# Kernel tuning notes

Measured on AMD Instinct MI355X. Metric: run time of the kernel, lower is better.

The kernel has to match this reference:

```python
import jax, jax.numpy as jnp
import numpy as np

BETA = 25.0  # torch nn.Softplus(beta=25.0)

def softplus_b(z):
    return jax.nn.softplus(BETA * z) / BETA

def setup_inputs() -> dict:
    key = jax.random.key(0)
    ks = jax.random.split(key, 9)
    B, H = 16384, 512
    def lin_init(kw, kb, out_f, in_f):
        bound = 1.0 / np.sqrt(in_f)
        W = jax.random.uniform(kw, (out_f, in_f), jnp.float32, -bound, bound)
        b = jax.random.uniform(kb, (out_f,), jnp.float32, -bound, bound)
        return W, b
    W0, b0 = lin_init(ks[1], ks[2], H, 4)
    W1, b1 = lin_init(ks[3], ks[4], H, H)
    W2, b2 = lin_init(ks[5], ks[6], H, H)
    W3, b3 = lin_init(ks[7], ks[8], 5, H)
    x = jax.random.normal(ks[0], (B, 4), jnp.float32)
    return {"x": x, "W0": W0, "b0": b0, "W1": W1, "b1": b1,
            "W2": W2, "b2": b2, "W3": W3, "b3": b3}

def reference(x, W0, b0, W1, b1, W2, b2, W3, b3):
    def net(z):  # (4,) -> (5,)
        h = softplus_b(W0 @ z + b0)
        h = softplus_b(W1 @ h + b1)
        h = softplus_b(W2 @ h + b2)
        return W3 @ h + b3

    def A_matrix(z):  # antisymmetrized Jacobian of first 4 outputs, (4,4)
        J = jax.jacrev(lambda p: net(p)[:4])(z)
        return J - J.T

    def point_trace(z):
        # T[i,j,k] = d A[i,j] / d z[k]; torch einsum('...ii') -> sum_j T[i,j,j]
        T = jax.jacfwd(A_matrix)(z)  # (4,4,4)
        return jnp.einsum('ijj->i', T)  # (4,)

    trace = jax.vmap(point_trace)(x)          # (B,4)
    u = jax.vmap(net)(x)                      # (B,5)
    return jnp.concatenate([trace, u[:, 4:5]], axis=1)  # (B,5)
```

## Files before the change

kernel.cpp:

```cpp
#include <hip/hip_runtime.h>
#include <math.h>

#define HDIM 512
#define NCH 16
#define BETA 25.0f
#define KV 1536

typedef unsigned short ushort_t;
typedef __attribute__((ext_vector_type(8))) short short8;
typedef __attribute__((ext_vector_type(4))) float f32x4;

__device__ __forceinline__ ushort_t f2bf(float f) {
    unsigned u = __float_as_uint(f);
    unsigned r = (u + 0x7fff + ((u >> 16) & 1)) >> 16;
    return (ushort_t)r;
}
__device__ __forceinline__ float bf2f(ushort_t b) {
    return __uint_as_float(((unsigned)b) << 16);
}
__device__ __forceinline__ void split_bf(float v, ushort_t& hi, ushort_t& lo) {
    hi = f2bf(v);
    lo = f2bf(v - bf2f(hi));
}

__device__ __forceinline__ void softplus_jet(float v, float& phi, float& s, float& pp) {
    float y = BETA * v;
    float e = expf(-fabsf(y));
    float inv = 1.0f / (1.0f + e);
    s = (y >= 0.0f) ? inv : e * inv;
    phi = (fmaxf(y, 0.0f) + log1pf(e)) * (1.0f / BETA);
    pp = BETA * s * (1.0f - s);
}

__device__ __forceinline__ void gl_lds16(const void* g, void* l) {
    __builtin_amdgcn_global_load_lds(
        (const __attribute__((address_space(1))) unsigned int*)g,
        (__attribute__((address_space(3))) unsigned int*)l, 16, 0, 0);
}

__global__ __launch_bounds__(256) void layer0_jet(
    const float* __restrict__ x, const float* __restrict__ W0,
    const float* __restrict__ b0, ushort_t* __restrict__ A0)
{
    __shared__ ushort_t sm[16 * 1024];
    int p = blockIdx.x, tid = threadIdx.x;
    float4 z = *reinterpret_cast<const float4*>(&x[p * 4]);
#pragma unroll
    for (int half = 0; half < 2; ++half) {
        int n = half * 256 + tid;
        float4 w = *reinterpret_cast<const float4*>(&W0[n * 4]);
        float v = fmaf(w.x, z.x, fmaf(w.y, z.y, fmaf(w.z, z.z, fmaf(w.w, z.w, b0[n]))));
        float phi, s, pp;
        softplus_jet(v, phi, s, pp);
        float wa[4] = {w.x, w.y, w.z, w.w};
        float o[16];
        o[0] = phi;
#pragma unroll
        for (int a = 0; a < 4; ++a) o[1 + a] = s * wa[a];
        int idx = 5;
#pragma unroll
        for (int a = 0; a < 4; ++a)
#pragma unroll
            for (int b = a; b < 4; ++b) { o[idx] = pp * wa[a] * wa[b]; ++idx; }
        o[15] = 0.0f;
#pragma unroll
        for (int c = 0; c < 16; ++c) {
            ushort_t hb, lb;
            split_bf(o[c], hb, lb);
            sm[c * 1024 + n] = hb;
            sm[c * 1024 + 512 + n] = lb;
        }
    }
    __syncthreads();
    uint4* d4 = reinterpret_cast<uint4*>(A0 + (size_t)p * 16 * 1024);
    const uint4* s4 = reinterpret_cast<const uint4*>(sm);
#pragma unroll
    for (int i = 0; i < 8; ++i) d4[tid + 256 * i] = s4[tid + 256 * i];
}

template<int EPI>
__global__ __launch_bounds__(256, 2) void gemm_jet(
    const ushort_t* __restrict__ Ag, const ushort_t* __restrict__ BT,
    const float* __restrict__ bias, ushort_t* __restrict__ Anext,
    float* __restrict__ Sout)
{
    __shared__ char smem[32768];
    ushort_t* Al = (ushort_t*)smem;
    ushort_t* Bl = (ushort_t*)(smem + 16384);
    float*    epi = (float*)smem;

    const int tid = threadIdx.x, wave = tid >> 6, lane = tid & 63;

    int nwg = gridDim.x;
    int bid = blockIdx.x;
    int q = nwg >> 3, r = nwg & 7;
    int xcd = bid & 7, i8 = bid >> 3;
    int logical = (xcd < r ? xcd * (q + 1) : r * (q + 1) + (xcd - r) * q) + i8;
    const int m0 = (logical >> 2) * 128;
    const int n0 = (logical & 3) * 128;
    const int wm = (wave >> 1) * 64, wn = (wave & 1) * 64;

    f32x4 acc[4][4] = {};

    const int sr = wave * 32 + (lane >> 3);
    const int sc = (lane & 7) * 8;

    for (int t = 0; t < KV / 64; ++t) {
        int k0 = t * 64;
        int ka = (k0 < 512) ? k0 : k0 - 512;
        __syncthreads();
#pragma unroll
        for (int i = 0; i < 4; ++i)
            gl_lds16(Ag + (size_t)(m0 + sr + i * 8) * 1024 + ka + sc,
                     Al + (wave * 32 + i * 8) * 64);
#pragma unroll
        for (int i = 0; i < 4; ++i)
            gl_lds16(BT + (size_t)(n0 + sr + i * 8) * KV + k0 + sc,
                     Bl + (wave * 32 + i * 8) * 64);
        __syncthreads();
        const int rA = lane & 15;
#pragma unroll
        for (int kk = 0; kk < 2; ++kk) {
            const int kc = kk * 32 + (lane >> 4) * 8;
            short8 af[4], bf[4];
#pragma unroll
            for (int mi = 0; mi < 4; ++mi)
                af[mi] = *(const short8*)&Al[(wm + mi * 16 + rA) * 64 + kc];
#pragma unroll
            for (int ni = 0; ni < 4; ++ni)
                bf[ni] = *(const short8*)&Bl[(wn + ni * 16 + rA) * 64 + kc];
#pragma unroll
            for (int mi = 0; mi < 4; ++mi)
#pragma unroll
                for (int ni = 0; ni < 4; ++ni)
                    acc[mi][ni] = __builtin_amdgcn_mfma_f32_16x16x32_bf16(
                        af[mi], bf[ni], acc[mi][ni], 0, 0, 0);
        }
    }

    const int pl = lane & 15, ph = lane >> 4;
#pragma unroll
    for (int h = 0; h < 2; ++h) {
        __syncthreads();
        if ((wave >> 1) == h) {
#pragma unroll
            for (int mi = 0; mi < 4; ++mi)
#pragma unroll
                for (int ni = 0; ni < 4; ++ni)
#pragma unroll
                    for (int rr = 0; rr < 4; ++rr)
                        epi[(mi * 16 + ph * 4 + rr) * 128 + wn + ni * 16 + pl] = acc[mi][ni][rr];
        }
        __syncthreads();
#pragma unroll
        for (int rep = 0; rep < 2; ++rep) {
            int idx = rep * 256 + tid;
            int n = idx & 127, pq = idx >> 7;
            const float* vp = &epi[pq * 16 * 128 + n];
            float v[15];
#pragma unroll
            for (int c = 0; c < 15; ++c) v[c] = vp[c * 128];
            float val = v[0] + bias[n0 + n];
            float phi, s, pp;
            softplus_jet(val, phi, s, pp);
            float o[16];
            o[0] = phi;
            float d[4];
#pragma unroll
            for (int a = 0; a < 4; ++a) { d[a] = v[1 + a]; o[1 + a] = s * d[a]; }
            int ix = 5;
#pragma unroll
            for (int a = 0; a < 4; ++a)
#pragma unroll
                for (int b = a; b < 4; ++b) { o[ix] = pp * d[a] * d[b] + s * v[ix]; ++ix; }
            o[15] = 0.0f;
            size_t prow = (size_t)(m0 >> 4) + h * 4 + pq;
            if (EPI == 1) {
                size_t rb = prow * 16 * 1024;
#pragma unroll
                for (int c = 0; c < 16; ++c) {
                    ushort_t hb, lb;
                    split_bf(o[c], hb, lb);
                    Anext[rb + (size_t)c * 1024 + n0 + n] = hb;
                    Anext[rb + (size_t)c * 1024 + 512 + n0 + n] = lb;
                }
            } else {
                float4* op = reinterpret_cast<float4*>(Sout + ((size_t)prow * 512 + n0 + n) * 16);
#pragma unroll
                for (int qq = 0; qq < 4; ++qq)
                    op[qq] = make_float4(o[4*qq], o[4*qq+1], o[4*qq+2], o[4*qq+3]);
            }
        }
    }
}

__global__ __launch_bounds__(256) void trace_kernel(
    const float* __restrict__ Sin, const float* __restrict__ W3,
    const float* __restrict__ b3, float* __restrict__ out, int npts)
{
    int wave = threadIdx.x >> 6;
    int lane = threadIdx.x & 63;
    int p = blockIdx.x * 4 + wave;
    if (p >= npts) return;
    const float* sp = Sin + (size_t)p * (HDIM * NCH);

    float hu[4][10];
#pragma unroll
    for (int m = 0; m < 4; ++m)
#pragma unroll
        for (int qq = 0; qq < 10; ++qq) hu[m][qq] = 0.0f;
    float u4 = 0.0f;

    for (int kk = 0; kk < 8; ++kk) {
        int k = kk * 64 + lane;
        const float* sk = sp + k * NCH;
        float4 s0 = *reinterpret_cast<const float4*>(&sk[0]);
        float4 s1 = *reinterpret_cast<const float4*>(&sk[4]);
        float4 s2 = *reinterpret_cast<const float4*>(&sk[8]);
        float4 s3 = *reinterpret_cast<const float4*>(&sk[12]);
        float hv[10] = {s1.y,s1.z,s1.w, s2.x,s2.y,s2.z,s2.w, s3.x,s3.y,s3.z};
        float w3m[5];
#pragma unroll
        for (int m = 0; m < 5; ++m) w3m[m] = W3[m * HDIM + k];
        u4 = fmaf(w3m[4], s0.x, u4);
#pragma unroll
        for (int m = 0; m < 4; ++m)
#pragma unroll
            for (int qq = 0; qq < 10; ++qq) hu[m][qq] = fmaf(w3m[m], hv[qq], hu[m][qq]);
    }

#pragma unroll
    for (int off = 32; off > 0; off >>= 1) {
#pragma unroll
        for (int m = 0; m < 4; ++m)
#pragma unroll
            for (int qq = 0; qq < 10; ++qq) hu[m][qq] += __shfl_xor(hu[m][qq], off, 64);
        u4 += __shfl_xor(u4, off, 64);
    }

    if (lane == 0) {
        const int Pm[4][4] = {{0,1,2,3},{1,4,5,6},{2,5,7,8},{3,6,8,9}};
        const int Pd[4] = {0, 4, 7, 9};
#pragma unroll
        for (int i = 0; i < 4; ++i) {
            float t1 = hu[i][Pd[0]] + hu[i][Pd[1]] + hu[i][Pd[2]] + hu[i][Pd[3]];
            float t2 = hu[0][Pm[0][i]] + hu[1][Pm[1][i]] + hu[2][Pm[2][i]] + hu[3][Pm[3][i]];
            out[p * 5 + i] = t1 - t2;
        }
        out[p * 5 + 4] = u4 + b3[4];
    }
}

__global__ void prep_B(const float* __restrict__ W1, const float* __restrict__ W2,
                       ushort_t* __restrict__ BT1, ushort_t* __restrict__ BT2)
{
    int tid = blockIdx.x * 256 + threadIdx.x;
    int l = tid >> 18;
    int i = tid & 262143;
    int n = i >> 9, k = i & 511;
    const float* W = l ? W2 : W1;
    ushort_t* BT = l ? BT2 : BT1;
    float v = W[i];
    ushort_t hb, lb;
    split_bf(v, hb, lb);
    size_t rr = (size_t)n * KV;
    BT[rr + k] = hb;
    BT[rr + 512 + k] = lb;
    BT[rr + 1024 + k] = hb;
}

extern "C" void kernel_launch(void* const* d_in, const int* in_sizes, int n_in,
                              void* d_out, int out_size, void* d_ws, size_t ws_size,
                              hipStream_t stream)
{
    const float* x  = (const float*)d_in[0];
    const float* W0 = (const float*)d_in[1];
    const float* b0 = (const float*)d_in[2];
    const float* W1 = (const float*)d_in[3];
    const float* b1 = (const float*)d_in[4];
    const float* W2 = (const float*)d_in[5];
    const float* b2 = (const float*)d_in[6];
    const float* W3 = (const float*)d_in[7];
    const float* b3 = (const float*)d_in[8];
    float* out = (float*)d_out;

    int B = in_sizes[0] / 4;

    ushort_t* BT1 = (ushort_t*)d_ws;
    ushort_t* BT2 = BT1 + 512 * KV;
    char* bufbase = (char*)(BT2 + 512 * KV);

    size_t avail = ws_size - 2ull * 512 * KV * sizeof(ushort_t);
    size_t per_pt = 2ull * 32768;
    int Pc = (int)(avail / per_pt) & ~7;
    if (Pc > 4096) Pc = 4096;
    if (Pc < 8) Pc = 8;

    ushort_t* A0 = (ushort_t*)bufbase;
    ushort_t* A1 = (ushort_t*)(bufbase + (size_t)Pc * 32768);
    float* S2 = (float*)A0;

    prep_B<<<2048, 256, 0, stream>>>(W1, W2, BT1, BT2);

    for (int base = 0; base < B; base += Pc) {
        int np = (B - base < Pc) ? (B - base) : Pc;
        layer0_jet<<<np, 256, 0, stream>>>(x + (size_t)base * 4, W0, b0, A0);
        int nwg = (np / 8) * 4;
        gemm_jet<1><<<nwg, 256, 0, stream>>>(A0, BT1, b1, A1, nullptr);
        gemm_jet<2><<<nwg, 256, 0, stream>>>(A1, BT2, b2, nullptr, S2);
        trace_kernel<<<(np + 3) / 4, 256, 0, stream>>>(S2, W3, b3, out + (size_t)base * 5, np);
    }
}
```

Measured before the change: 1.443 ms.

## Use 256x256 tile GEMM with 8 waves and multi-stage LDS pipelining

Replaces the 128x128, 4-wave GEMM with a 256x256-tile kernel using 8 waves and a 4-slot LDS ring buffer. Global-to-LDS loads for future k-steps are issued while MFMAs run, with fine-grained barriers and setprio around the compute. The chunk size is raised so fewer host-loop iterations are needed. This targets load latency and per-tile overhead, at the cost of 128KB LDS per block and more complex synchronisation.

```diff
diff --git a/kernel.cpp b/kernel.cpp
--- a/kernel.cpp
+++ b/kernel.cpp
@@ -5,6 +5,7 @@
 #define NCH 16
 #define BETA 25.0f
 #define KV 1536
+#define NKH 48
 
 typedef unsigned short ushort_t;
 typedef __attribute__((ext_vector_type(8))) short short8;
@@ -79,87 +80,131 @@
 }
 
 template<int EPI>
-__global__ __launch_bounds__(256, 2) void gemm_jet(
+__global__ __launch_bounds__(512, 2) void gemm_jet8(
     const ushort_t* __restrict__ Ag, const ushort_t* __restrict__ BT,
     const float* __restrict__ bias, ushort_t* __restrict__ Anext,
     float* __restrict__ Sout)
 {
-    __shared__ char smem[32768];
-    ushort_t* Al = (ushort_t*)smem;
-    ushort_t* Bl = (ushort_t*)(smem + 16384);
+    __shared__ char smem[131072];
+    ushort_t* Asl = (ushort_t*)smem;
+    ushort_t* Bsl = (ushort_t*)(smem + 65536);
     float*    epi = (float*)smem;
 
-    const int tid = threadIdx.x, wave = tid >> 6, lane = tid & 63;
-
-    int nwg = gridDim.x;
-    int bid = blockIdx.x;
+    const int tid = threadIdx.x;
+    const int wave = tid >> 6, lane = tid & 63;
+    const int wr = wave >> 2, wc = wave & 3;
+
+    int nwg = gridDim.x, bid = blockIdx.x;
     int q = nwg >> 3, r = nwg & 7;
     int xcd = bid & 7, i8 = bid >> 3;
     int logical = (xcd < r ? xcd * (q + 1) : r * (q + 1) + (xcd - r) * q) + i8;
-    const int m0 = (logical >> 2) * 128;
-    const int n0 = (logical & 3) * 128;
-    const int wm = (wave >> 1) * 64, wn = (wave & 1) * 64;
-
-    f32x4 acc[4][4] = {};
-
-    const int sr = wave * 32 + (lane >> 3);
-    const int sc = (lane & 7) * 8;
-
-    for (int t = 0; t < KV / 64; ++t) {
-        int k0 = t * 64;
+    const int mt = logical >> 1;
+    const int m0 = mt * 256;
+    const int n0 = (logical & 1) * 256;
+
+    const int s_w2 = wave * 2;
+    const int s_r  = lane >> 2;
+    const int s_c  = (lane & 3) * 8;
+
+    f32x4 acc[8][4] = {};
+
+    auto stageA = [&](int g) {
+        if (g >= NKH) g -= NKH;
+        const int slot = g & 3;
+        int k0 = g * 32;
         int ka = (k0 < 512) ? k0 : k0 - 512;
-        __syncthreads();
-#pragma unroll
-        for (int i = 0; i < 4; ++i)
-            gl_lds16(Ag + (size_t)(m0 + sr + i * 8) * 1024 + ka + sc,
-                     Al + (wave * 32 + i * 8) * 64);
-#pragma unroll
-        for (int i = 0; i < 4; ++i)
-            gl_lds16(BT + (size_t)(n0 + sr + i * 8) * KV + k0 + sc,
-                     Bl + (wave * 32 + i * 8) * 64);
-        __syncthreads();
-        const int rA = lane & 15;
-#pragma unroll
-        for (int kk = 0; kk < 2; ++kk) {
-            const int kc = kk * 32 + (lane >> 4) * 8;
-            short8 af[4], bf[4];
+#pragma unroll
+        for (int rr = 0; rr < 2; ++rr) {
+            int row = (s_w2 + rr) * 16 + s_r;
+            gl_lds16(Ag + (size_t)(m0 + row) * 1024 + ka + s_c,
+                     Asl + slot * 8192 + (s_w2 + rr) * 512);
+        }
+    };
+    auto stageB = [&](int g) {
+        if (g >= NKH) g -= NKH;
+        const int slot = g & 3;
+        int k0 = g * 32;
+#pragma unroll
+        for (int rr = 0; rr < 2; ++rr) {
+            int row = (s_w2 + rr) * 16 + s_r;
+            gl_lds16(BT + (size_t)(n0 + row) * KV + k0 + s_c,
+                     Bsl + slot * 8192 + (s_w2 + rr) * 512);
+        }
+    };
+
+    stageA(0); stageB(0); stageA(1); stageB(1); stageA(2); stageB(2);
+    asm volatile("s_waitcnt vmcnt(8)" ::: "memory");
+    __builtin_amdgcn_s_barrier();
+    asm volatile("" ::: "memory");
+
+    const int rA = lane & 15;
+    const int kc = (lane >> 4) * 8;
+
+    for (int j = 0; j < 12; ++j) {
+        short8 bf[4];
+#pragma unroll
+        for (int p = 0; p < 8; ++p) {
+            const int kh = p >> 1, qm = p & 1;
+            const int slot = kh;
+            const ushort_t* Ab = Asl + slot * 8192;
+            const ushort_t* Bb = Bsl + slot * 8192;
+            short8 af[4];
 #pragma unroll
             for (int mi = 0; mi < 4; ++mi)
-                af[mi] = *(const short8*)&Al[(wm + mi * 16 + rA) * 64 + kc];
-#pragma unroll
-            for (int ni = 0; ni < 4; ++ni)
-                bf[ni] = *(const short8*)&Bl[(wn + ni * 16 + rA) * 64 + kc];
+                af[mi] = *(const short8*)&Ab[(wr * 128 + qm * 64 + mi * 16 + rA) * 32 + kc];
+            if (qm == 0) {
+#pragma unroll
+                for (int ni = 0; ni < 4; ++ni)
+                    bf[ni] = *(const short8*)&Bb[(wc * 64 + ni * 16 + rA) * 32 + kc];
+            }
+            if (qm == 0) stageA(4 * j + 3 + kh); else stageB(4 * j + 3 + kh);
+            if (qm == 1) asm volatile("s_waitcnt vmcnt(8)" ::: "memory");
+            asm volatile("" ::: "memory");
+            __builtin_amdgcn_s_barrier();
+            asm volatile("s_waitcnt lgkmcnt(0)" ::: "memory");
+            __builtin_amdgcn_sched_barrier(0);
+            __builtin_amdgcn_s_setprio(1);
 #pragma unroll
             for (int mi = 0; mi < 4; ++mi)
 #pragma unroll
                 for (int ni = 0; ni < 4; ++ni)
-                    acc[mi][ni] = __builtin_amdgcn_mfma_f32_16x16x32_bf16(
-                        af[mi], bf[ni], acc[mi][ni], 0, 0, 0);
-        }
-    }
+                    acc[qm * 4 + mi][ni] = __builtin_amdgcn_mfma_f32_16x16x32_bf16(
+                        af[mi], bf[ni], acc[qm * 4 + mi][ni], 0, 0, 0);
+            __builtin_amdgcn_s_setprio(0);
+            asm volatile("" ::: "memory");
+            __builtin_amdgcn_s_barrier();
+            asm volatile("" ::: "memory");
+        }
+    }
+
+    asm volatile("s_waitcnt vmcnt(0)" ::: "memory");
+    __builtin_amdgcn_s_barrier();
+    asm volatile("" ::: "memory");
 
     const int pl = lane & 15, ph = lane >> 4;
 #pragma unroll
     for (int h = 0; h < 2; ++h) {
-        __syncthreads();
-        if ((wave >> 1) == h) {
-#pragma unroll
-            for (int mi = 0; mi < 4; ++mi)
+        if (h) { asm volatile("" ::: "memory"); __builtin_amdgcn_s_barrier(); }
+        if (wr == h) {
+#pragma unroll
+            for (int am = 0; am < 8; ++am)
 #pragma unroll
                 for (int ni = 0; ni < 4; ++ni)
 #pragma unroll
                     for (int rr = 0; rr < 4; ++rr)
-                        epi[(mi * 16 + ph * 4 + rr) * 128 + wn + ni * 16 + pl] = acc[mi][ni][rr];
-        }
-        __syncthreads();
-#pragma unroll
-        for (int rep = 0; rep < 2; ++rep) {
-            int idx = rep * 256 + tid;
-            int n = idx & 127, pq = idx >> 7;
-            const float* vp = &epi[pq * 16 * 128 + n];
+                        epi[(am * 16 + ph * 4 + rr) * 256 + wc * 64 + ni * 16 + pl] = acc[am][ni][rr];
+        }
+        asm volatile("" ::: "memory");
+        __builtin_amdgcn_s_barrier();
+        asm volatile("" ::: "memory");
+#pragma unroll
+        for (int rep = 0; rep < 4; ++rep) {
+            int idx = rep * 512 + tid;
+            int n = idx & 255, pq = idx >> 8;
+            const float* vp = &epi[pq * 16 * 256 + n];
             float v[15];
 #pragma unroll
-            for (int c = 0; c < 15; ++c) v[c] = vp[c * 128];
+            for (int c = 0; c < 15; ++c) v[c] = vp[c * 256];
             float val = v[0] + bias[n0 + n];
             float phi, s, pp;
             softplus_jet(val, phi, s, pp);
@@ -174,7 +219,7 @@
 #pragma unroll
                 for (int b = a; b < 4; ++b) { o[ix] = pp * d[a] * d[b] + s * v[ix]; ++ix; }
             o[15] = 0.0f;
-            size_t prow = (size_t)(m0 >> 4) + h * 4 + pq;
+            size_t prow = (size_t)mt * 16 + h * 8 + pq;
             if (EPI == 1) {
                 size_t rb = prow * 16 * 1024;
 #pragma unroll
@@ -292,9 +337,9 @@
 
     size_t avail = ws_size - 2ull * 512 * KV * sizeof(ushort_t);
     size_t per_pt = 2ull * 32768;
-    int Pc = (int)(avail / per_pt) & ~7;
-    if (Pc > 4096) Pc = 4096;
-    if (Pc < 8) Pc = 8;
+    int Pc = (int)(avail / per_pt) & ~15;
+    if (Pc > 16384) Pc = 16384;
+    if (Pc < 16) Pc = 16;
 
     ushort_t* A0 = (ushort_t*)bufbase;
     ushort_t* A1 = (ushort_t*)(bufbase + (size_t)Pc * 32768);
@@ -305,9 +350,9 @@
     for (int base = 0; base < B; base += Pc) {
         int np = (B - base < Pc) ? (B - base) : Pc;
         layer0_jet<<<np, 256, 0, stream>>>(x + (size_t)base * 4, W0, b0, A0);
-        int nwg = (np / 8) * 4;
-        gemm_jet<1><<<nwg, 256, 0, stream>>>(A0, BT1, b1, A1, nullptr);
-        gemm_jet<2><<<nwg, 256, 0, stream>>>(A1, BT2, b2, nullptr, S2);
+        int nwg = (np / 16) * 2;
+        gemm_jet8<1><<<nwg, 512, 0, stream>>>(A0, BT1, b1, A1, nullptr);
+        gemm_jet8<2><<<nwg, 512, 0, stream>>>(A1, BT2, b2, nullptr, S2);
         trace_kernel<<<(np + 3) / 4, 256, 0, stream>>>(S2, W3, b3, out + (size_t)base * 5, np);
     }
 }
```

After: 1.391 ms. -3.6%, faster.
